# Performance work log

Hardware: AMD Instinct MI355X
Metric: run time of the kernel (lower is better)

## Reference

```python
import jax, jax.numpy as jnp
import numpy as np

B, M, IN, HID, A = 4096, 64, 3, 128, 64
D = 50.0                       # waveguide_bound
H_CONST = 5.0
PMAX = 10.0 ** (30 / 10 - 3)   # = 1.0 (30 dBm in Watts)
C_LIGHT = 3.0e8
FC = 6.0e9
DELTA_MIN = (C_LIGHT / FC) / 2.0  # 0.025
ALPHA = 0.2                    # LeakyReLU slope


def setup_inputs() -> dict:
    key = jax.random.key(0)
    ks = jax.random.split(key, 9)
    s = lambda k, sh: (jax.random.normal(k, sh, jnp.float32) * 0.1)
    return {
        "users": jax.random.normal(ks[0], (B, M, IN), jnp.float32),
        "W1": s(ks[1], (IN, HID)),    # GAT layer 1 projection (applied as h @ W)
        "a1": s(ks[2], (2 * HID,)),   # GAT layer 1 attention vector
        "W2": s(ks[3], (HID, HID)),   # GAT layer 2 projection
        "a2": s(ks[4], (2 * HID,)),
        "mw1": s(ks[5], (HID, 32)),   # MLP Linear(hidden, 32)
        "mb1": jnp.zeros((32,), jnp.float32),
        "mw2": s(ks[6], (32, 2 * A)), # MLP Linear(32, 2*num_antennas)
        "mb2": jnp.zeros((2 * A,), jnp.float32),
    }


def gat_layer(h, W, a):
    # Wh: [B, M, d]
    Wh = h @ W
    d = W.shape[1]
    # e[b,i,j] = leakyrelu( cat(Wh_i, Wh_j) . a ) = leakyrelu( Wh_i.a[:d] + Wh_j.a[d:] )
    si = Wh @ a[:d]          # [B, M]
    sj = Wh @ a[d:]          # [B, M]
    e = jax.nn.leaky_relu(si[:, :, None] + sj[:, None, :], ALPHA)  # [B, M, M]
    attn = jax.nn.softmax(e, axis=-1)  # softmax over neighbors j (dropout p=0 -> identity)
    h_prime = jnp.einsum('bij,bjd->bid', attn, Wh)
    return jax.nn.elu(h_prime)


def reference(users, W1, a1, W2, a2, mw1, mb1, mw2, mb2):
    h = gat_layer(users, W1, a1)
    h = gat_layer(h, W2, a2)
    pooled = jnp.max(h, axis=1)                      # [B, hidden]
    readout = jax.nn.relu(pooled @ mw1 + mb1) @ mw2 + mb2  # [B, 2A]
    raw_delta, raw_power = readout[:, :A], readout[:, A:]
    eps = 1e-6
    raw_delta = jax.nn.relu(raw_delta) + eps
    raw_power = jax.nn.relu(raw_power) + eps
    Bmax = 2.0 * D - (A - 1) * DELTA_MIN
    delta = Bmax * raw_delta / (jnp.sum(raw_delta, axis=1, keepdims=True) + eps)
    power = PMAX * raw_power / (jnp.sum(raw_power, axis=1, keepdims=True) + eps)
    return power, delta
```

## Files before the change

### kernel.cpp

```cpp
#include <hip/hip_runtime.h>

#define NBATCH 4096
#define OUT2 (NBATCH * 64)

typedef _Float16 f16;
typedef __attribute__((ext_vector_type(8))) _Float16 f16x8;
typedef __attribute__((ext_vector_type(4))) _Float16 f16x4;
typedef __attribute__((ext_vector_type(4))) float f32x4;

__device__ __forceinline__ float lrelu(float x) { return x > 0.0f ? x : 0.2f * x; }
__device__ __forceinline__ float elu1(float x)  { return x > 0.0f ? x : __expf(x) - 1.0f; }

__global__ void prep(const float* __restrict__ W2, const float* __restrict__ W1,
                     const float* __restrict__ a1, const float* __restrict__ a2,
                     f16* __restrict__ w2b, float* __restrict__ w1a, f16* __restrict__ w2ab) {
    const int flat = blockIdx.x * 256 + threadIdx.x;
    const int slot = flat >> 3, j = flat & 7;
    const int F2T = slot >> 8, kf = (slot >> 6) & 3, ln = slot & 63;
    const int lq = ln >> 4, lr = ln & 15;
    w2b[flat] = (f16)W2[(kf * 32 + lq * 8 + j) * 128 + F2T * 16 + lr];
    if (flat < 2048) {
        const int ks = flat >> 9, ln2 = (flat >> 3) & 63, jj = flat & 7;
        const int k = ks * 32 + ((ln2 >> 4) & 3) * 8 + jj;
        const int n = ln2 & 15;
        float v = 0.f;
        if (n < 2) {
            const float* av = a2 + n * 128;
            for (int f2 = 0; f2 < 128; ++f2) v = fmaf(W2[k * 128 + f2], av[f2], v);
        }
        w2ab[flat] = (f16)v;
    }
    if (flat >= 16381) {
        const int c = flat - 16381;
        float si = 0.f, sj = 0.f;
        for (int f = 0; f < 128; ++f) {
            const float w = W1[c * 128 + f];
            si = fmaf(w, a1[f], si);
            sj = fmaf(w, a1[128 + f], sj);
        }
        w1a[c] = si; w1a[3 + c] = sj;
    }
}

__global__ __launch_bounds__(64, 2)
void gat_kernel(const float* __restrict__ users,
                const float* __restrict__ W1,
                const f16* __restrict__ w2b,
                const float* __restrict__ w1a,
                const f16* __restrict__ w2ab,
                const float* __restrict__ mw1,
                const float* __restrict__ mb1,
                const float* __restrict__ mw2,
                const float* __restrict__ mb2,
                float* __restrict__ out)
{
    const int b = blockIdx.x;
    const int lane = threadIdx.x;
    const int lr = lane & 15;
    const int lq = lane >> 4;

    __shared__ __align__(16) char smem[9344];
    f16*   sMain = (f16*)smem;
    float* sSi   = (float*)(smem + 8192);
    float* sSj   = (float*)(smem + 8448);
    float* sPool = (float*)(smem + 8704);
    float* sHid  = (float*)(smem + 9216);

    const float* u = users + b * 192;

    {
        const float x = u[lane * 3], y = u[lane * 3 + 1], z = u[lane * 3 + 2];
        sSi[lane] = fmaf(x, w1a[0], fmaf(y, w1a[1], z * w1a[2]));
        sSj[lane] = fmaf(x, w1a[3], fmaf(y, w1a[4], z * w1a[5]));
    }
    __syncthreads();

    f16x8 bfr[4];
    float inv1[4];
    {
        float sjv[16];
        *(float4*)&sjv[0]  = *(const float4*)&sSj[lq * 8];
        *(float4*)&sjv[4]  = *(const float4*)&sSj[lq * 8 + 4];
        *(float4*)&sjv[8]  = *(const float4*)&sSj[32 + lq * 8];
        *(float4*)&sjv[12] = *(const float4*)&sSj[32 + lq * 8 + 4];
        f16x8 ap[4][2];
        #pragma unroll
        for (int mt = 0; mt < 4; ++mt) {
            const float si = sSi[mt * 16 + lr];
            float lsum = 0.f;
            #pragma unroll
            for (int jj = 0; jj < 8; ++jj) {
                float p = __expf(lrelu(si + sjv[jj]));
                f16 ph = (f16)p; lsum += (float)ph; ap[mt][0][jj] = ph;
                p = __expf(lrelu(si + sjv[8 + jj]));
                ph = (f16)p; lsum += (float)ph; ap[mt][1][jj] = ph;
            }
            lsum += __shfl_xor(lsum, 16, 64);
            lsum += __shfl_xor(lsum, 32, 64);
            inv1[mt] = 1.0f / lsum;
        }
        f16x8 af2[2];
        #pragma unroll
        for (int ks = 0; ks < 2; ++ks) {
            #pragma unroll
            for (int jj = 0; jj < 8; ++jj) {
                const int node = ks * 32 + lq * 8 + jj;
                af2[ks][jj] = (lr < 3) ? (f16)u[node * 3 + lr] : (f16)0.f;
            }
        }
        #pragma unroll
        for (int nt = 0; nt < 4; ++nt) {
            f32x4 d1 = (f32x4){0.f, 0.f, 0.f, 0.f};
            d1 = __builtin_amdgcn_mfma_f32_16x16x32_f16(af2[0], ap[nt][0], d1, 0, 0, 0);
            d1 = __builtin_amdgcn_mfma_f32_16x16x32_f16(af2[1], ap[nt][1], d1, 0, 0, 0);
            const float c0 = __shfl(d1[0], lr, 64);
            const float c1 = __shfl(d1[1], lr, 64);
            const float c2 = __shfl(d1[2], lr, 64);
            #pragma unroll
            for (int jj = 0; jj < 8; ++jj) bfr[nt][jj] = (f16)0.f;
            if (lq == 0) {
                bfr[nt][0] = (f16)c0; bfr[nt][1] = (f16)c1; bfr[nt][2] = (f16)c2;
            }
        }
    }

    f16x8 hf[4][4];
    #pragma unroll
    for (int h = 0; h < 2; ++h) {
        __syncthreads();
        #pragma unroll
        for (int ftl = 0; ftl < 4; ++ftl) {
            f16x8 af3;
            #pragma unroll
            for (int jj = 0; jj < 8; ++jj) af3[jj] = (f16)0.f;
            if (lq == 0) {
                #pragma unroll
                for (int jj = 0; jj < 3; ++jj)
                    af3[jj] = (f16)W1[jj * 128 + (h * 4 + ftl) * 16 + lr];
            }
            #pragma unroll
            for (int nt = 0; nt < 4; ++nt) {
                f32x4 acc = (f32x4){0.f, 0.f, 0.f, 0.f};
                acc = __builtin_amdgcn_mfma_f32_16x16x32_f16(af3, bfr[nt], acc, 0, 0, 0);
                f16x4 hv;
                #pragma unroll
                for (int r = 0; r < 4; ++r) hv[r] = (f16)elu1(acc[r] * inv1[nt]);
                const int n = nt * 16 + lr;
                const int gg = 2 * ftl + (lq >> 1);
                *(f16x4*)&sMain[n * 64 + ((gg ^ (n & 7)) << 3) + ((lq & 1) * 4)] = hv;
            }
        }
        __syncthreads();
        #pragma unroll
        for (int nt = 0; nt < 4; ++nt) {
            const int n = nt * 16 + lr;
            #pragma unroll
            for (int ksl = 0; ksl < 2; ++ksl)
                hf[nt][h * 2 + ksl] =
                    *(const f16x8*)&sMain[n * 64 + (((ksl * 4 + lq) ^ (n & 7)) << 3)];
        }
    }

    {
        f32x4 sacc[4];
        #pragma unroll
        for (int mt = 0; mt < 4; ++mt) sacc[mt] = (f32x4){0.f, 0.f, 0.f, 0.f};
        #pragma unroll
        for (int ks = 0; ks < 4; ++ks) {
            f16x8 bsw = *(const f16x8*)(w2ab + (ks * 64 + lane) * 8);
            #pragma unroll
            for (int mt = 0; mt < 4; ++mt)
                sacc[mt] = __builtin_amdgcn_mfma_f32_16x16x32_f16(hf[mt][ks], bsw, sacc[mt], 0, 0, 0);
        }
        __syncthreads();
        if (lr < 2) {
            float* dst = (lr == 0) ? sSi : sSj;
            #pragma unroll
            for (int mt = 0; mt < 4; ++mt)
                #pragma unroll
                for (int r = 0; r < 4; ++r)
                    dst[mt * 16 + lq * 4 + r] = sacc[mt][r];
        }
    }
    __syncthreads();

    f16x8 bp[4][2];
    float inv2[4];
    {
        float sjv[16];
        *(float4*)&sjv[0]  = *(const float4*)&sSj[lq * 8];
        *(float4*)&sjv[4]  = *(const float4*)&sSj[lq * 8 + 4];
        *(float4*)&sjv[8]  = *(const float4*)&sSj[32 + lq * 8];
        *(float4*)&sjv[12] = *(const float4*)&sSj[32 + lq * 8 + 4];
        #pragma unroll
        for (int mt = 0; mt < 4; ++mt) {
            const float si = sSi[mt * 16 + lr];
            float lsum = 0.f;
            #pragma unroll
            for (int jj = 0; jj < 8; ++jj) {
                float p = __expf(lrelu(si + sjv[jj]));
                f16 ph = (f16)p; lsum += (float)ph; bp[mt][0][jj] = ph;
                p = __expf(lrelu(si + sjv[8 + jj]));
                ph = (f16)p; lsum += (float)ph; bp[mt][1][jj] = ph;
            }
            lsum += __shfl_xor(lsum, 16, 64);
            lsum += __shfl_xor(lsum, 32, 64);
            inv2[mt] = 1.0f / lsum;
        }
    }

    #pragma unroll 1
    for (int ft = 0; ft < 8; ++ft) {
        f16x8 bw2[4];
        #pragma unroll
        for (int kf = 0; kf < 4; ++kf)
            bw2[kf] = *(const f16x8*)(w2b + ((ft * 4 + kf) * 64 + lane) * 8);
        #pragma unroll
        for (int nt = 0; nt < 4; ++nt) {
            f32x4 acc = (f32x4){0.f, 0.f, 0.f, 0.f};
            #pragma unroll
            for (int kf = 0; kf < 4; ++kf)
                acc = __builtin_amdgcn_mfma_f32_16x16x32_f16(hf[nt][kf], bw2[kf], acc, 0, 0, 0);
            const int gg = nt * 2 + (lq >> 1);
            f16x4 hv;
            #pragma unroll
            for (int r = 0; r < 4; ++r) hv[r] = (f16)acc[r];
            *(f16x4*)&sMain[lr * 64 + ((gg ^ (lr & 7)) << 3) + ((lq & 1) * 4)] = hv;
        }
        __syncthreads();

        f16x8 bh0 = *(const f16x8*)&sMain[lr * 64 + ((lq ^ (lr & 7)) << 3)];
        f16x8 bh1 = *(const f16x8*)&sMain[lr * 64 + (((4 + lq) ^ (lr & 7)) << 3)];
        f32x4 mx4 = (f32x4){-1e30f, -1e30f, -1e30f, -1e30f};
        #pragma unroll
        for (int mt = 0; mt < 4; ++mt) {
            f32x4 acc = (f32x4){0.f, 0.f, 0.f, 0.f};
            acc = __builtin_amdgcn_mfma_f32_16x16x32_f16(bh0, bp[mt][0], acc, 0, 0, 0);
            acc = __builtin_amdgcn_mfma_f32_16x16x32_f16(bh1, bp[mt][1], acc, 0, 0, 0);
            #pragma unroll
            for (int r = 0; r < 4; ++r)
                mx4[r] = fmaxf(mx4[r], acc[r] * inv2[mt]);
        }
        #pragma unroll
        for (int m = 1; m < 16; m <<= 1) {
            #pragma unroll
            for (int r = 0; r < 4; ++r)
                mx4[r] = fmaxf(mx4[r], __shfl_xor(mx4[r], m, 64));
        }
        if (lr == 0) {
            float4 pv;
            pv.x = elu1(mx4[0]); pv.y = elu1(mx4[1]);
            pv.z = elu1(mx4[2]); pv.w = elu1(mx4[3]);
            *(float4*)&sPool[ft * 16 + lq * 4] = pv;
        }
        __syncthreads();
    }

    {
        const int o = lane & 31, hh = lane >> 5;
        float s0 = 0.f;
        #pragma unroll 8
        for (int kk = 0; kk < 64; ++kk) {
            const int c = hh * 64 + kk;
            s0 = fmaf(sPool[c], mw1[c * 32 + o], s0);
        }
        s0 += __shfl_xor(s0, 32, 64);
        if (lane < 32) sHid[lane] = fmaxf(s0 + mb1[o], 0.0f);
    }
    __syncthreads();
    {
        float sA = mb2[lane], sB = mb2[64 + lane];
        #pragma unroll 8
        for (int q = 0; q < 32; ++q) {
            const float wA = mw2[q * 128 + lane];
            const float wB = mw2[q * 128 + 64 + lane];
            const float h0 = sHid[q];
            sA = fmaf(h0, wA, sA);  sB = fmaf(h0, wB, sB);
        }
        float rA = fmaxf(sA, 0.0f) + 1e-6f, rB = fmaxf(sB, 0.0f) + 1e-6f;
        float uA = rA, uB = rB;
        #pragma unroll
        for (int m = 1; m < 64; m <<= 1) {
            uA += __shfl_xor(uA, m, 64);  uB += __shfl_xor(uB, m, 64);
        }
        out[b * 64 + lane]        = rB / (uB + 1e-6f);
        out[OUT2 + b * 64 + lane] = 98.425f * rA / (uA + 1e-6f);
    }
}

extern "C" void kernel_launch(void* const* d_in, const int* in_sizes, int n_in,
                              void* d_out, int out_size, void* d_ws, size_t ws_size,
                              hipStream_t stream) {
    const float* users = (const float*)d_in[0];
    const float* W1    = (const float*)d_in[1];
    const float* a1    = (const float*)d_in[2];
    const float* W2    = (const float*)d_in[3];
    const float* a2    = (const float*)d_in[4];
    const float* mw1   = (const float*)d_in[5];
    const float* mb1   = (const float*)d_in[6];
    const float* mw2   = (const float*)d_in[7];
    const float* mb2   = (const float*)d_in[8];
    float* out = (float*)d_out;

    f16*   w2b  = (f16*)d_ws;
    float* w1a  = (float*)((char*)d_ws + 32768);
    f16*   w2ab = (f16*)((char*)d_ws + 32800);

    prep<<<64, 256, 0, stream>>>(W2, W1, a1, a2, w2b, w1a, w2ab);
    gat_kernel<<<NBATCH, 64, 0, stream>>>(users, W1, w2b, w1a, w2ab,
                                          mw1, mb1, mw2, mb2, out);
}
```

Baseline: 114.0 us.

## Double-buffer layer-2 projection tiles and fold softmax normalization into attention weights

The layer-2 loop now double-buffers the shared-memory tile, so the projection for the next feature tile is computed while the current tile's attention product runs. This removes one barrier per iteration. Softmax weights are normalized before the f16 conversion, which drops the per-element inverse multiplies. The MFMA operands are swapped so the max-pool reduces within a lane plus two shuffles instead of four shuffle rounds. The normalized f16 probabilities change rounding slightly, and the second buffer uses more LDS.

Measured after the change: 114.9 us. About the same (+0.8%).

```diff
diff --git a/kernel.cpp b/kernel.cpp
--- a/kernel.cpp
+++ b/kernel.cpp
@@ -8,7 +8,7 @@
 typedef __attribute__((ext_vector_type(4))) _Float16 f16x4;
 typedef __attribute__((ext_vector_type(4))) float f32x4;
 
-__device__ __forceinline__ float lrelu(float x) { return x > 0.0f ? x : 0.2f * x; }
+__device__ __forceinline__ float lrelu(float x) { return fmaxf(x, 0.2f * x); }
 __device__ __forceinline__ float elu1(float x)  { return x > 0.0f ? x : __expf(x) - 1.0f; }
 
 __global__ void prep(const float* __restrict__ W2, const float* __restrict__ W1,
@@ -76,7 +76,6 @@
     __syncthreads();
 
     f16x8 bfr[4];
-    float inv1[4];
     {
         float sjv[16];
         *(float4*)&sjv[0]  = *(const float4*)&sSj[lq * 8];
@@ -87,17 +86,25 @@
         #pragma unroll
         for (int mt = 0; mt < 4; ++mt) {
             const float si = sSi[mt * 16 + lr];
+            float pv[16];
             float lsum = 0.f;
             #pragma unroll
             for (int jj = 0; jj < 8; ++jj) {
-                float p = __expf(lrelu(si + sjv[jj]));
-                f16 ph = (f16)p; lsum += (float)ph; ap[mt][0][jj] = ph;
-                p = __expf(lrelu(si + sjv[8 + jj]));
-                ph = (f16)p; lsum += (float)ph; ap[mt][1][jj] = ph;
+                const float t0 = si + sjv[jj];
+                const float t1 = si + sjv[8 + jj];
+                const float p0 = __expf(lrelu(t0));
+                const float p1 = __expf(lrelu(t1));
+                pv[jj] = p0; pv[8 + jj] = p1;
+                lsum += p0 + p1;
             }
             lsum += __shfl_xor(lsum, 16, 64);
             lsum += __shfl_xor(lsum, 32, 64);
-            inv1[mt] = 1.0f / lsum;
+            const float inv = 1.0f / lsum;
+            #pragma unroll
+            for (int jj = 0; jj < 8; ++jj) {
+                ap[mt][0][jj] = (f16)(pv[jj] * inv);
+                ap[mt][1][jj] = (f16)(pv[8 + jj] * inv);
+            }
         }
         f16x8 af2[2];
         #pragma unroll
@@ -144,7 +151,7 @@
                 acc = __builtin_amdgcn_mfma_f32_16x16x32_f16(af3, bfr[nt], acc, 0, 0, 0);
                 f16x4 hv;
                 #pragma unroll
-                for (int r = 0; r < 4; ++r) hv[r] = (f16)elu1(acc[r] * inv1[nt]);
+                for (int r = 0; r < 4; ++r) hv[r] = (f16)elu1(acc[r]);
                 const int n = nt * 16 + lr;
                 const int gg = 2 * ftl + (lq >> 1);
                 *(f16x4*)&sMain[n * 64 + ((gg ^ (n & 7)) << 3) + ((lq & 1) * 4)] = hv;
@@ -185,7 +192,6 @@
     __syncthreads();
 
     f16x8 bp[4][2];
-    float inv2[4];
     {
         float sjv[16];
         *(float4*)&sjv[0]  = *(const float4*)&sSj[lq * 8];
@@ -195,64 +201,91 @@
         #pragma unroll
         for (int mt = 0; mt < 4; ++mt) {
             const float si = sSi[mt * 16 + lr];
+            float pv[16];
             float lsum = 0.f;
             #pragma unroll
             for (int jj = 0; jj < 8; ++jj) {
-                float p = __expf(lrelu(si + sjv[jj]));
-                f16 ph = (f16)p; lsum += (float)ph; bp[mt][0][jj] = ph;
-                p = __expf(lrelu(si + sjv[8 + jj]));
-                ph = (f16)p; lsum += (float)ph; bp[mt][1][jj] = ph;
+                const float t0 = si + sjv[jj];
+                const float t1 = si + sjv[8 + jj];
+                const float p0 = __expf(lrelu(t0));
+                const float p1 = __expf(lrelu(t1));
+                pv[jj] = p0; pv[8 + jj] = p1;
+                lsum += p0 + p1;
             }
             lsum += __shfl_xor(lsum, 16, 64);
             lsum += __shfl_xor(lsum, 32, 64);
-            inv2[mt] = 1.0f / lsum;
-        }
-    }
+            const float inv = 1.0f / lsum;
+            #pragma unroll
+            for (int jj = 0; jj < 8; ++jj) {
+                bp[mt][0][jj] = (f16)(pv[jj] * inv);
+                bp[mt][1][jj] = (f16)(pv[8 + jj] * inv);
+            }
+        }
+    }
+
+    int fst[4];
+    #pragma unroll
+    for (int nt = 0; nt < 4; ++nt) {
+        const int gg = nt * 2 + (lq >> 1);
+        fst[nt] = lr * 64 + ((gg ^ (lr & 7)) << 3) + ((lq & 1) * 4);
+    }
+    const int er0 = lr * 64 + ((lq ^ (lr & 7)) << 3);
+    const int er1 = lr * 64 + (((4 + lq) ^ (lr & 7)) << 3);
+
+    {
+        f16x8 bw2[4];
+        #pragma unroll
+        for (int kf = 0; kf < 4; ++kf)
+            bw2[kf] = *(const f16x8*)(w2b + ((0 * 4 + kf) * 64 + lane) * 8);
+        #pragma unroll
+        for (int nt = 0; nt < 4; ++nt) {
+            f32x4 acc = (f32x4){0.f, 0.f, 0.f, 0.f};
+            #pragma unroll
+            for (int kf = 0; kf < 4; ++kf)
+                acc = __builtin_amdgcn_mfma_f32_16x16x32_f16(hf[nt][kf], bw2[kf], acc, 0, 0, 0);
+            f16x4 hv;
+            #pragma unroll
+            for (int r = 0; r < 4; ++r) hv[r] = (f16)acc[r];
+            *(f16x4*)&sMain[fst[nt]] = hv;
+        }
+    }
+    __syncthreads();
 
     #pragma unroll 1
     for (int ft = 0; ft < 8; ++ft) {
-        f16x8 bw2[4];
-        #pragma unroll
-        for (int kf = 0; kf < 4; ++kf)
-            bw2[kf] = *(const f16x8*)(w2b + ((ft * 4 + kf) * 64 + lane) * 8);
-        #pragma unroll
-        for (int nt = 0; nt < 4; ++nt) {
-            f32x4 acc = (f32x4){0.f, 0.f, 0.f, 0.f};
+        f16* rb = sMain + ((ft & 1) << 10);
+        if (ft < 7) {
+            f16* wb = sMain + (((ft + 1) & 1) << 10);
+            f16x8 bw2[4];
             #pragma unroll
             for (int kf = 0; kf < 4; ++kf)
-                acc = __builtin_amdgcn_mfma_f32_16x16x32_f16(hf[nt][kf], bw2[kf], acc, 0, 0, 0);
-            const int gg = nt * 2 + (lq >> 1);
-            f16x4 hv;
-            #pragma unroll
-            for (int r = 0; r < 4; ++r) hv[r] = (f16)acc[r];
-            *(f16x4*)&sMain[lr * 64 + ((gg ^ (lr & 7)) << 3) + ((lq & 1) * 4)] = hv;
-        }
-        __syncthreads();
-
-        f16x8 bh0 = *(const f16x8*)&sMain[lr * 64 + ((lq ^ (lr & 7)) << 3)];
-        f16x8 bh1 = *(const f16x8*)&sMain[lr * 64 + (((4 + lq) ^ (lr & 7)) << 3)];
-        f32x4 mx4 = (f32x4){-1e30f, -1e30f, -1e30f, -1e30f};
+                bw2[kf] = *(const f16x8*)(w2b + (((ft + 1) * 4 + kf) * 64 + lane) * 8);
+            #pragma unroll
+            for (int nt = 0; nt < 4; ++nt) {
+                f32x4 acc = (f32x4){0.f, 0.f, 0.f, 0.f};
+                #pragma unroll
+                for (int kf = 0; kf < 4; ++kf)
+                    acc = __builtin_amdgcn_mfma_f32_16x16x32_f16(hf[nt][kf], bw2[kf], acc, 0, 0, 0);
+                f16x4 hv;
+                #pragma unroll
+                for (int r = 0; r < 4; ++r) hv[r] = (f16)acc[r];
+                *(f16x4*)&wb[fst[nt]] = hv;
+            }
+        }
+
+        f16x8 bh0 = *(const f16x8*)&rb[er0];
+        f16x8 bh1 = *(const f16x8*)&rb[er1];
+        float mx = -1e30f;
         #pragma unroll
         for (int mt = 0; mt < 4; ++mt) {
             f32x4 acc = (f32x4){0.f, 0.f, 0.f, 0.f};
-            acc = __builtin_amdgcn_mfma_f32_16x16x32_f16(bh0, bp[mt][0], acc, 0, 0, 0);
-            acc = __builtin_amdgcn_mfma_f32_16x16x32_f16(bh1, bp[mt][1], acc, 0, 0, 0);
-            #pragma unroll
-            for (int r = 0; r < 4; ++r)
-                mx4[r] = fmaxf(mx4[r], acc[r] * inv2[mt]);
-        }
-        #pragma unroll
-        for (int m = 1; m < 16; m <<= 1) {
-            #pragma unroll
-            for (int r = 0; r < 4; ++r)
-                mx4[r] = fmaxf(mx4[r], __shfl_xor(mx4[r], m, 64));
-        }
-        if (lr == 0) {
-            float4 pv;
-            pv.x = elu1(mx4[0]); pv.y = elu1(mx4[1]);
-            pv.z = elu1(mx4[2]); pv.w = elu1(mx4[3]);
-            *(float4*)&sPool[ft * 16 + lq * 4] = pv;
-        }
+            acc = __builtin_amdgcn_mfma_f32_16x16x32_f16(bp[mt][0], bh0, acc, 0, 0, 0);
+            acc = __builtin_amdgcn_mfma_f32_16x16x32_f16(bp[mt][1], bh1, acc, 0, 0, 0);
+            mx = fmaxf(mx, fmaxf(fmaxf(acc[0], acc[1]), fmaxf(acc[2], acc[3])));
+        }
+        mx = fmaxf(mx, __shfl_xor(mx, 16, 64));
+        mx = fmaxf(mx, __shfl_xor(mx, 32, 64));
+        if (lane < 16) sPool[ft * 16 + lane] = elu1(mx);
         __syncthreads();
     }
 
```
